# Kernel tuning notes

Hardware: AMD Instinct MI355X
Metric: run time of the kernel (lower is better)

The kernel has to match this reference:

```python
import jax, jax.numpy as jnp
import numpy as np

B, S, HID = 2, 2048, 2048
H, KVH, D = 8, 1, 256
RQ, RK, RV = 6, 2, 2
SCALING = 256 ** -0.5  # query_pre_attn_scalar
SOFTCAP = 50.0
NEG = -2.3819763e38


def setup_inputs() -> dict:
    key = jax.random.key(0)
    ks = jax.random.split(key, 9)
    hidden_states = jax.random.normal(ks[0], (B, S, HID), dtype=jnp.float32)
    # RoPE tables (split-half convention, matching torch view_as_complex path)
    inv_freq = 1.0 / (10000.0 ** (np.arange(0, D, 2, dtype=np.float32) / D))
    t = np.arange(S, dtype=np.float32)
    ang = np.outer(t, inv_freq)  # [S, D/2]
    freqs_cos = jnp.asarray(np.cos(ang))
    freqs_sin = jnp.asarray(np.sin(ang))
    causal = jnp.tril(jnp.ones((S, S), dtype=bool))
    mask = jnp.where(causal, 0.0, NEG)[None, None].astype(jnp.float32)
    kv_write_indices = jnp.arange(S, dtype=jnp.int32)
    sc = lambda fan_in: 1.0 / np.sqrt(fan_in)
    W_A_q = jax.random.normal(ks[1], (H * RQ, HID), dtype=jnp.float32) * sc(HID)
    W_A_k = jax.random.normal(ks[2], (KVH * RK, HID), dtype=jnp.float32) * sc(HID)
    W_A_v = jax.random.normal(ks[3], (KVH * RV, HID), dtype=jnp.float32) * sc(HID)
    W_B_q = jax.random.normal(ks[4], (RQ * D, HID), dtype=jnp.float32) * sc(HID)
    W_B_k = jax.random.normal(ks[5], (RK * D, HID), dtype=jnp.float32) * sc(HID)
    W_B_v = jax.random.normal(ks[6], (RV * D, HID), dtype=jnp.float32) * sc(HID)
    W_o = jax.random.normal(ks[7], (HID, H * D), dtype=jnp.float32) * sc(H * D)
    return {"hidden_states": hidden_states, "freqs_cos": freqs_cos,
            "freqs_sin": freqs_sin, "mask": mask,
            "kv_write_indices": kv_write_indices,
            "W_A_q": W_A_q, "W_A_k": W_A_k, "W_A_v": W_A_v,
            "W_B_q": W_B_q, "W_B_k": W_B_k, "W_B_v": W_B_v, "W_o": W_o}


def _rope(x, cos, sin):
    # x: [B,S,R,D]; cos/sin: [S,D/2]. Split-half rotation.
    x1, x2 = jnp.split(x, 2, axis=-1)
    c = cos[None, :, None, :]
    s = sin[None, :, None, :]
    return jnp.concatenate([x1 * c - x2 * s, x1 * s + x2 * c], axis=-1)


def reference(hidden_states, freqs_cos, freqs_sin, mask, kv_write_indices,
              W_A_q, W_A_k, W_A_v, W_B_q, W_B_k, W_B_v, W_o):
    b, s, _ = hidden_states.shape
    A_q = (hidden_states @ W_A_q.T).reshape(b, s, H, RQ)
    A_k = (hidden_states @ W_A_k.T).reshape(b, s, KVH, RK)
    A_v = (hidden_states @ W_A_v.T).reshape(b, s, KVH, RV)
    B_q = (hidden_states @ W_B_q.T).reshape(b, s, RQ, D)
    B_k = (hidden_states @ W_B_k.T).reshape(b, s, RK, D)
    B_v = (hidden_states @ W_B_v.T).reshape(b, s, RV, D)
    B_q = _rope(B_q, freqs_cos, freqs_sin)
    B_k = _rope(B_k, freqs_cos, freqs_sin)
    # Prefill: kv_write_indices = arange(s), so cache slices equal current factors.
    # GQA expansion of KV A-factors to all heads.
    A_k = jnp.repeat(A_k, H // KVH, axis=2)  # [b,s,H,RK]
    A_v = jnp.repeat(A_v, H // KVH, axis=2)
    # Reconstruct full-rank Q/K/V from TPA factors (1/rank per TPA definition).
    q = jnp.einsum('bshr,bsrd->bshd', A_q, B_q) / RQ
    k = jnp.einsum('bshr,bsrd->bshd', A_k, B_k) / RK
    v = jnp.einsum('bshr,bsrd->bshd', A_v, B_v) / RV
    scores = jnp.einsum('bqhd,bkhd->bhqk', q, k) * SCALING
    scores = jnp.tanh(scores / SOFTCAP) * SOFTCAP
    scores = scores + mask
    probs = jax.nn.softmax(scores.astype(jnp.float32), axis=-1).astype(q.dtype)
    out = jnp.einsum('bhqk,bkhd->bqhd', probs, v).reshape(b, s, H * D)
    return out @ W_o.T
```

## Files before the change

kernel.cpp:

```cpp
#include <hip/hip_runtime.h>
#include <hip/hip_bf16.h>
#include <stdint.h>

typedef __bf16 bf16;
typedef __bf16 bf16x8 __attribute__((ext_vector_type(8)));
typedef float  f32x4  __attribute__((ext_vector_type(4)));

static constexpr int S_LEN = 2048;
static constexpr int HIDN  = 2048;
static constexpr int BATCH = 2;
static constexpr int MTOT  = BATCH * S_LEN;
static constexpr int NH    = 8;
static constexpr int DH    = 256;
static constexpr int NPAD  = 2688;
static constexpr float QSCALE = 0.0625f / 6.0f;

__device__ __forceinline__ void gload16(const bf16* g, const bf16* l) {
  __builtin_amdgcn_global_load_lds(
      (const __attribute__((address_space(1))) void*)g,
      (__attribute__((address_space(3))) void*)l, 16, 0, 0);
}

__global__ void cast_x_kernel(const float* __restrict__ in, bf16* __restrict__ out) {
  int i = blockIdx.x * blockDim.x + threadIdx.x;
  const float4* p = reinterpret_cast<const float4*>(in) + 2 * (size_t)i;
  float4 a = p[0], b = p[1];
  bf16x8 o;
  o[0]=(bf16)a.x; o[1]=(bf16)a.y; o[2]=(bf16)a.z; o[3]=(bf16)a.w;
  o[4]=(bf16)b.x; o[5]=(bf16)b.y; o[6]=(bf16)b.z; o[7]=(bf16)b.w;
  reinterpret_cast<bf16x8*>(out)[i] = o;
}

__global__ void cast_w_kernel(const float* __restrict__ Wq, const float* __restrict__ Wk,
                              const float* __restrict__ Wv, const float* __restrict__ Bq,
                              const float* __restrict__ Bk, const float* __restrict__ Bv,
                              const float* __restrict__ Wo, bf16* __restrict__ Wcat,
                              bf16* __restrict__ Wob) {
  int row = blockIdx.x;
  int c = threadIdx.x * 8;
  const float* src = nullptr;
  bf16* dst;
  if (row < NPAD) {
    dst = Wcat + (size_t)row * HIDN;
    if      (row <   48) src = Wq + (size_t)row        * HIDN;
    else if (row <   50) src = Wk + (size_t)(row-  48) * HIDN;
    else if (row <   52) src = Wv + (size_t)(row-  50) * HIDN;
    else if (row < 1588) src = Bq + (size_t)(row-  52) * HIDN;
    else if (row < 2100) src = Bk + (size_t)(row-1588) * HIDN;
    else if (row < 2612) src = Bv + (size_t)(row-2100) * HIDN;
  } else {
    dst = Wob + (size_t)(row - NPAD) * HIDN;
    src = Wo + (size_t)(row - NPAD) * HIDN;
  }
  bf16x8 o;
  if (src) {
    const float4* p = reinterpret_cast<const float4*>(src + c);
    float4 a = p[0], b = p[1];
    o[0]=(bf16)a.x; o[1]=(bf16)a.y; o[2]=(bf16)a.z; o[3]=(bf16)a.w;
    o[4]=(bf16)b.x; o[5]=(bf16)b.y; o[6]=(bf16)b.z; o[7]=(bf16)b.w;
  } else {
    #pragma unroll
    for (int j = 0; j < 8; ++j) o[j] = (bf16)0.f;
  }
  *reinterpret_cast<bf16x8*>(dst + c) = o;
}

__launch_bounds__(256)
__global__ void gemm_bt_kernel(const bf16* __restrict__ A, const bf16* __restrict__ Bt,
                               float* __restrict__ C, int K, int N) {
  __shared__ __align__(16) bf16 As[2][128 * 64];
  __shared__ __align__(16) bf16 Bs[2][128 * 64];
  const int t = threadIdx.x;
  const int lane = t & 63, wid = t >> 6;
  const int g = lane >> 4, c16 = lane & 15;
  const int nwg = (int)(gridDim.x * gridDim.y);
  int flat = (int)(blockIdx.y * gridDim.x + blockIdx.x);
  flat = (flat & 7) * (nwg >> 3) + (flat >> 3);
  const int bxs = flat % (int)gridDim.x, bys = flat / (int)gridDim.x;
  const int rowA0 = bys * 128, rowB0 = bxs * 128;
  const int wrow = (wid >> 1) * 64, wcol = (wid & 1) * 64;
  const int srow = (lane >> 3), sunit = lane & 7;
  const int sgx = (sunit ^ (srow & 7)) * 8;
  const int rswz = c16 & 7;
  f32x4 z = {0.f, 0.f, 0.f, 0.f};
  f32x4 acc[4][4];
  #pragma unroll
  for (int m = 0; m < 4; ++m)
    #pragma unroll
    for (int n = 0; n < 4; ++n) acc[m][n] = z;

  auto stage = [&](int buf, int kt) {
    #pragma unroll
    for (int i = 0; i < 4; ++i) {
      int r0 = wid * 32 + i * 8;
      gload16(A + (size_t)(rowA0 + r0 + srow) * K + kt + sgx, &As[buf][r0 * 64]);
      gload16(Bt + (size_t)(rowB0 + r0 + srow) * K + kt + sgx, &Bs[buf][r0 * 64]);
    }
  };

  const int nk = K >> 6;
  stage(0, 0);
  __syncthreads();
  for (int ti = 0; ti < nk; ++ti) {
    const int cb = ti & 1;
    if (ti + 1 < nk) stage(cb ^ 1, (ti + 1) * 64);
    #pragma unroll
    for (int ks = 0; ks < 2; ++ks) {
      bf16x8 af[4], bfr[4];
      #pragma unroll
      for (int m = 0; m < 4; ++m)
        af[m] = *reinterpret_cast<const bf16x8*>(
            &As[cb][(wrow + m*16 + c16) * 64 + ((ks*4 + g) ^ rswz) * 8]);
      #pragma unroll
      for (int n = 0; n < 4; ++n)
        bfr[n] = *reinterpret_cast<const bf16x8*>(
            &Bs[cb][(wcol + n*16 + c16) * 64 + ((ks*4 + g) ^ rswz) * 8]);
      __builtin_amdgcn_s_setprio(1);
      #pragma unroll
      for (int m = 0; m < 4; ++m)
        #pragma unroll
        for (int n = 0; n < 4; ++n)
          acc[m][n] = __builtin_amdgcn_mfma_f32_16x16x32_bf16(af[m], bfr[n], acc[m][n], 0, 0, 0);
      __builtin_amdgcn_s_setprio(0);
    }
    __syncthreads();
  }
  #pragma unroll
  for (int m = 0; m < 4; ++m)
    #pragma unroll
    for (int n = 0; n < 4; ++n)
      #pragma unroll
      for (int r = 0; r < 4; ++r) {
        int row = rowA0 + wrow + m*16 + g*4 + r;
        int col = rowB0 + wcol + n*16 + c16;
        C[(size_t)row * N + col] = acc[m][n][r];
      }
}

__global__ void qkv_kernel(const float* __restrict__ P, const float* __restrict__ fcos,
                           const float* __restrict__ fsin, bf16* __restrict__ qat,
                           bf16* __restrict__ kat, bf16* __restrict__ vT) {
  const int m = blockIdx.x;
  const int b = m >> 11, s = m & 2047;
  const int d = threadIdx.x;
  __shared__ float Aq[48]; __shared__ float Ak[2]; __shared__ float Av[2];
  const float* Prow = P + (size_t)m * NPAD;
  if (d < 48) Aq[d] = Prow[d];
  else if (d < 50) Ak[d - 48] = Prow[d];
  else if (d < 52) Av[d - 50] = Prow[d];
  __syncthreads();
  const int dh = d & 127;
  const float co = fcos[s * 128 + dh], si = fsin[s * 128 + dh];
  const bool lo = (d < 128);
  float rq[6];
  #pragma unroll
  for (int r = 0; r < 6; ++r) {
    const float* Bq = Prow + 52 + r * 256;
    float x  = Bq[d];
    float xp = Bq[lo ? d + 128 : d - 128];
    rq[r] = lo ? (x * co - xp * si) : (xp * si + x * co);
  }
  #pragma unroll
  for (int h = 0; h < 8; ++h) {
    float a = 0.f;
    #pragma unroll
    for (int r = 0; r < 6; ++r) a += Aq[h * 6 + r] * rq[r];
    qat[((size_t)(b * 8 + h) * S_LEN + s) * DH + d] = (bf16)(a * QSCALE);
  }
  float ka = 0.f;
  #pragma unroll
  for (int r = 0; r < 2; ++r) {
    const float* Bk = Prow + 1588 + r * 256;
    float x  = Bk[d];
    float xp = Bk[lo ? d + 128 : d - 128];
    float rk = lo ? (x * co - xp * si) : (xp * si + x * co);
    ka += Ak[r] * rk;
  }
  kat[((size_t)b * S_LEN + s) * DH + d] = (bf16)(ka * 0.5f);
  float va = 0.f;
  #pragma unroll
  for (int r = 0; r < 2; ++r) va += Av[r] * Prow[2100 + r * 256 + d];
  vT[((size_t)b * DH + d) * S_LEN + s] = (bf16)(va * 0.5f);
}

__launch_bounds__(512)
__global__ void attn_kernel(const bf16* __restrict__ qat, const bf16* __restrict__ kat,
                            const bf16* __restrict__ vT, bf16* __restrict__ O) {
  const int pr = (int)blockIdx.x;
  const int bh = (int)blockIdx.y;
  const int b = bh >> 3, h8 = bh & 7;
  const int t = threadIdx.x, lane = t & 63, w = t >> 6;
  const int g = lane >> 4, c16 = lane & 15;
  const int rw = w & 3, hf = w >> 2;
  __shared__ __align__(16) bf16 Kb[2][64 * 256];
  __shared__ __align__(16) bf16 Vb[2][256 * 64];
  __shared__ __align__(16) bf16 Pl[8][16 * 40];
  __shared__ f32x4 Lc[4][64];
  float* Fc = (float*)&Kb[0][0];

  const int ks_r = lane >> 5, ks_x = lane & 31;
  const int vs_r = lane >> 3, vs_x = lane & 7;
  const size_t kbase = (size_t)b * S_LEN * DH;
  const size_t vbase = (size_t)b * DH * S_LEN;

  auto stage = [&](int buf, int j0) {
    #pragma unroll
    for (int i = 0; i < 4; ++i) {
      int lr = w * 8 + i * 2 + ks_r;
      int gx = ks_x ^ (lr & 7);
      gload16(kat + kbase + (size_t)(j0 + lr) * DH + gx * 8,
              &Kb[buf][(w * 8 + i * 2) * 256]);
    }
    #pragma unroll
    for (int i = 0; i < 4; ++i) {
      int lr = w * 32 + i * 8 + vs_r;
      int gx = vs_x ^ (lr & 7);
      gload16(vT + vbase + (size_t)lr * S_LEN + j0 + gx * 8,
              &Vb[buf][(w * 32 + i * 8) * 64]);
    }
  };

  f32x4 z = {0.f, 0.f, 0.f, 0.f};
  const int kswz = c16 & 7;

  #pragma unroll 1
  for (int half = 0; half < 2; ++half) {
    const int qt = half ? pr : 31 - pr;
    const int q0 = qt * 64;
    const int rowg0 = q0 + rw * 16 + g * 4;

    bf16x8 qf[8];
    {
      const bf16* qrow = qat + ((size_t)bh * S_LEN + q0 + rw * 16 + c16) * DH;
      #pragma unroll
      for (int kf = 0; kf < 8; ++kf)
        qf[kf] = *reinterpret_cast<const bf16x8*>(qrow + kf * 32 + g * 8);
    }
    f32x4 accO[16];
    #pragma unroll
    for (int i = 0; i < 16; ++i) accO[i] = z;
    float lr4[4] = {0.f, 0.f, 0.f, 0.f};

    const int nst = qt + 1;
    stage(0, 0);
    __syncthreads();

    for (int ts = 0; ts < nst; ++ts) {
      const int cb = ts & 1, nb = cb ^ 1;
      const int j0 = ts * 64;
      if (ts + 1 < nst) stage(nb, j0 + 64);

      f32x4 sc[2];
      #pragma unroll
      for (int nt = 0; nt < 2; ++nt) {
        f32x4 a = z;
        const int rk = hf * 32 + nt * 16 + c16;
        __builtin_amdgcn_s_setprio(1);
        #pragma unroll
        for (int kf = 0; kf < 8; ++kf) {
          bf16x8 kb = *reinterpret_cast<const bf16x8*>(
              &Kb[cb][rk * 256 + ((kf * 4 + g) ^ kswz) * 8]);
          a = __builtin_amdgcn_mfma_f32_16x16x32_bf16(qf[kf], kb, a, 0, 0, 0);
        }
        __builtin_amdgcn_s_setprio(0);
        sc[nt] = a;
      }
      #pragma unroll
      for (int nt = 0; nt < 2; ++nt) {
        int col = j0 + hf * 32 + nt * 16 + c16;
        #pragma unroll
        for (int r = 0; r < 4; ++r) {
          float x = sc[nt][r];
          float e2 = __expf(x * 0.04f);
          float p = (col <= rowg0 + r)
                      ? __expf(-100.f * __frcp_rn(e2 + 1.f))
                      : 0.f;
          lr4[r] += p;
          Pl[w][(g * 4 + r) * 40 + nt * 16 + c16] = (bf16)p;
        }
      }
      bf16x8 pa = *reinterpret_cast<const bf16x8*>(&Pl[w][c16 * 40 + g * 8]);
      __builtin_amdgcn_s_setprio(1);
      #pragma unroll
      for (int dt = 0; dt < 16; ++dt) {
        int vrow = dt * 16 + c16;
        bf16x8 vb = *reinterpret_cast<const bf16x8*>(
            &Vb[cb][vrow * 64 + ((hf * 4 + g) ^ (vrow & 7)) * 8]);
        accO[dt] = __builtin_amdgcn_mfma_f32_16x16x32_bf16(pa, vb, accO[dt], 0, 0, 0);
      }
      __builtin_amdgcn_s_setprio(0);
      __syncthreads();
    }

    if (hf == 1) {
      #pragma unroll
      for (int dt = 0; dt < 16; ++dt)
        #pragma unroll
        for (int r = 0; r < 4; ++r)
          Fc[rw * 4096 + (g * 4 + r) * 256 + dt * 16 + c16] = accO[dt][r];
      f32x4 lv = {lr4[0], lr4[1], lr4[2], lr4[3]};
      Lc[rw][lane] = lv;
    }
    __syncthreads();
    if (hf == 0) {
      f32x4 lo = Lc[rw][lane];
      #pragma unroll
      for (int r = 0; r < 4; ++r) lr4[r] += lo[r];
      #pragma unroll
      for (int dt = 0; dt < 16; ++dt)
        #pragma unroll
        for (int r = 0; r < 4; ++r)
          accO[dt][r] += Fc[rw * 4096 + (g * 4 + r) * 256 + dt * 16 + c16];
      #pragma unroll
      for (int r = 0; r < 4; ++r) {
        float l = lr4[r];
        l += __shfl_xor(l, 1);
        l += __shfl_xor(l, 2);
        l += __shfl_xor(l, 4);
        l += __shfl_xor(l, 8);
        float inv = 1.f / l;
        #pragma unroll
        for (int dt = 0; dt < 16; ++dt)
          O[((size_t)b * S_LEN + rowg0 + r) * (size_t)(NH * DH) + h8 * DH + dt * 16 + c16] =
              (bf16)(accO[dt][r] * inv);
      }
    }
    __syncthreads();
  }
}

extern "C" void kernel_launch(void* const* d_in, const int* in_sizes, int n_in,
                              void* d_out, int out_size, void* d_ws, size_t ws_size,
                              hipStream_t stream) {
  (void)in_sizes; (void)n_in; (void)out_size; (void)ws_size;
  const float* hs   = (const float*)d_in[0];
  const float* fcos = (const float*)d_in[1];
  const float* fsin = (const float*)d_in[2];
  const float* Wq = (const float*)d_in[5];
  const float* Wk = (const float*)d_in[6];
  const float* Wv = (const float*)d_in[7];
  const float* Bq = (const float*)d_in[8];
  const float* Bk = (const float*)d_in[9];
  const float* Bv = (const float*)d_in[10];
  const float* Wo = (const float*)d_in[11];

  char* ws = (char*)d_ws;
  size_t off = 0;
  auto alloc = [&](size_t bytes) {
    void* p = ws + off;
    off += (bytes + 255) & ~(size_t)255;
    return p;
  };
  bf16*  Xbf  = (bf16*) alloc((size_t)MTOT * HIDN * 2);
  bf16*  Wcat = (bf16*) alloc((size_t)NPAD * HIDN * 2);
  bf16*  Wob  = (bf16*) alloc((size_t)HIDN * HIDN * 2);
  float* P    = (float*)alloc((size_t)MTOT * NPAD * 4);
  bf16*  qat  = (bf16*) alloc((size_t)BATCH * NH * S_LEN * DH * 2);
  bf16*  kat  = (bf16*) alloc((size_t)BATCH * S_LEN * DH * 2);
  bf16*  vT   = (bf16*) alloc((size_t)BATCH * DH * S_LEN * 2);
  bf16*  Oat  = (bf16*) alloc((size_t)MTOT * NH * DH * 2);
  float* out  = (float*)d_out;

  cast_x_kernel<<<dim3(MTOT * HIDN / 8 / 256), dim3(256), 0, stream>>>(hs, Xbf);
  cast_w_kernel<<<dim3(NPAD + HIDN), dim3(256), 0, stream>>>(Wq, Wk, Wv, Bq, Bk, Bv, Wo, Wcat, Wob);
  gemm_bt_kernel<<<dim3(NPAD / 128, MTOT / 128), dim3(256), 0, stream>>>(Xbf, Wcat, P, HIDN, NPAD);
  qkv_kernel<<<dim3(MTOT), dim3(256), 0, stream>>>(P, fcos, fsin, qat, kat, vT);
  attn_kernel<<<dim3(16, BATCH * NH), dim3(512), 0, stream>>>(qat, kat, vT, Oat);
  gemm_bt_kernel<<<dim3(HIDN / 128, MTOT / 128), dim3(256), 0, stream>>>(Oat, Wob, out, HIDN, HIDN);
}
```

Baseline: 230.6 us.

## Restructure attention to 32x32 MFMA tiles with single-buffer 256-thread blocks

Rewrites the attention kernel so each block handles one 64-row query tile with 4 waves using 32x32x16 MFMAs instead of 16x16x32. P is moved between lanes with cross-half shuffles rather than an LDS round trip. The K/V double buffering is dropped in favour of a single buffer, and the grid is flattened to 512 blocks ordered longest-first, with launch bounds set for 2 blocks per CU. This aims to cut LDS traffic, remove the paired-tile scheduling, and raise occupancy, at the cost of no longer overlapping loads with compute inside a block.

Result: slower. 248.8 us (+7.9%).

```diff
diff --git a/kernel.cpp b/kernel.cpp
--- a/kernel.cpp
+++ b/kernel.cpp
@@ -5,6 +5,9 @@
 typedef __bf16 bf16;
 typedef __bf16 bf16x8 __attribute__((ext_vector_type(8)));
 typedef float  f32x4  __attribute__((ext_vector_type(4)));
+typedef float  f32x16 __attribute__((ext_vector_type(16)));
+typedef unsigned int u32;
+typedef u32 u32x4 __attribute__((ext_vector_type(4)));
 
 static constexpr int S_LEN = 2048;
 static constexpr int HIDN  = 2048;
@@ -183,149 +186,140 @@
   vT[((size_t)b * DH + d) * S_LEN + s] = (bf16)(va * 0.5f);
 }
 
-__launch_bounds__(512)
+__launch_bounds__(256, 2)
 __global__ void attn_kernel(const bf16* __restrict__ qat, const bf16* __restrict__ kat,
                             const bf16* __restrict__ vT, bf16* __restrict__ O) {
-  const int pr = (int)blockIdx.x;
-  const int bh = (int)blockIdx.y;
+  const int f = (int)blockIdx.x;
+  int qt, bh;
+  if (f < 256) { qt = 31 - (f & 31); bh = f >> 5; }
+  else         { int g2 = f - 256; qt = g2 & 31; bh = 8 + (g2 >> 5); }
   const int b = bh >> 3, h8 = bh & 7;
   const int t = threadIdx.x, lane = t & 63, w = t >> 6;
-  const int g = lane >> 4, c16 = lane & 15;
-  const int rw = w & 3, hf = w >> 2;
-  __shared__ __align__(16) bf16 Kb[2][64 * 256];
-  __shared__ __align__(16) bf16 Vb[2][256 * 64];
-  __shared__ __align__(16) bf16 Pl[8][16 * 40];
-  __shared__ f32x4 Lc[4][64];
-  float* Fc = (float*)&Kb[0][0];
-
-  const int ks_r = lane >> 5, ks_x = lane & 31;
-  const int vs_r = lane >> 3, vs_x = lane & 7;
+  const int l31 = lane & 31, hi = lane >> 5;
+  const int rg = w >> 1, hf = w & 1;
+  const int q0 = qt * 64;
+
+  __shared__ __align__(16) bf16 Kb[64 * 256];
+  __shared__ __align__(16) bf16 Vb[256 * 64];
+  __shared__ float Lh[2][32];
+  __shared__ float Li[2][32];
+
+  const int qrow = q0 + rg * 32 + l31;
+  bf16x8 qf[16];
+  {
+    const bf16* qp = qat + ((size_t)bh * S_LEN + qrow) * DH + hi * 8;
+    #pragma unroll
+    for (int kf = 0; kf < 16; ++kf)
+      qf[kf] = *reinterpret_cast<const bf16x8*>(qp + kf * 16);
+  }
+  f32x16 acc[8];
+  #pragma unroll
+  for (int dt = 0; dt < 8; ++dt)
+    #pragma unroll
+    for (int e = 0; e < 16; ++e) acc[dt][e] = 0.f;
+  float lsum = 0.f;
+
   const size_t kbase = (size_t)b * S_LEN * DH;
   const size_t vbase = (size_t)b * DH * S_LEN;
-
-  auto stage = [&](int buf, int j0) {
-    #pragma unroll
-    for (int i = 0; i < 4; ++i) {
-      int lr = w * 8 + i * 2 + ks_r;
-      int gx = ks_x ^ (lr & 7);
-      gload16(kat + kbase + (size_t)(j0 + lr) * DH + gx * 8,
-              &Kb[buf][(w * 8 + i * 2) * 256]);
-    }
-    #pragma unroll
-    for (int i = 0; i < 4; ++i) {
-      int lr = w * 32 + i * 8 + vs_r;
-      int gx = vs_x ^ (lr & 7);
-      gload16(vT + vbase + (size_t)lr * S_LEN + j0 + gx * 8,
-              &Vb[buf][(w * 32 + i * 8) * 64]);
-    }
-  };
-
-  f32x4 z = {0.f, 0.f, 0.f, 0.f};
-  const int kswz = c16 & 7;
-
-  #pragma unroll 1
-  for (int half = 0; half < 2; ++half) {
-    const int qt = half ? pr : 31 - pr;
-    const int q0 = qt * 64;
-    const int rowg0 = q0 + rw * 16 + g * 4;
-
-    bf16x8 qf[8];
-    {
-      const bf16* qrow = qat + ((size_t)bh * S_LEN + q0 + rw * 16 + c16) * DH;
-      #pragma unroll
-      for (int kf = 0; kf < 8; ++kf)
-        qf[kf] = *reinterpret_cast<const bf16x8*>(qrow + kf * 32 + g * 8);
-    }
-    f32x4 accO[16];
-    #pragma unroll
-    for (int i = 0; i < 16; ++i) accO[i] = z;
-    float lr4[4] = {0.f, 0.f, 0.f, 0.f};
-
-    const int nst = qt + 1;
-    stage(0, 0);
+  const int krow_rd = hf * 32 + l31;
+  const int kswz = l31 & 7;
+
+  for (int ts = 0; ts <= qt; ++ts) {
+    const int j0 = ts * 64;
+    #pragma unroll
+    for (int i = 0; i < 8; ++i) {
+      int kr = i * 8 + (t >> 5);
+      gload16(kat + kbase + (size_t)(j0 + kr) * DH + ((t & 31) ^ (kr & 7)) * 8,
+              &Kb[(i * 256 + w * 64) * 8]);
+      int vr = i * 32 + (t >> 3);
+      gload16(vT + vbase + (size_t)vr * S_LEN + j0 + ((t & 7) ^ (vr & 7)) * 8,
+              &Vb[(i * 256 + w * 64) * 8]);
+    }
     __syncthreads();
 
-    for (int ts = 0; ts < nst; ++ts) {
-      const int cb = ts & 1, nb = cb ^ 1;
-      const int j0 = ts * 64;
-      if (ts + 1 < nst) stage(nb, j0 + 64);
-
-      f32x4 sc[2];
-      #pragma unroll
-      for (int nt = 0; nt < 2; ++nt) {
-        f32x4 a = z;
-        const int rk = hf * 32 + nt * 16 + c16;
-        __builtin_amdgcn_s_setprio(1);
-        #pragma unroll
-        for (int kf = 0; kf < 8; ++kf) {
-          bf16x8 kb = *reinterpret_cast<const bf16x8*>(
-              &Kb[cb][rk * 256 + ((kf * 4 + g) ^ kswz) * 8]);
-          a = __builtin_amdgcn_mfma_f32_16x16x32_bf16(qf[kf], kb, a, 0, 0, 0);
-        }
-        __builtin_amdgcn_s_setprio(0);
-        sc[nt] = a;
+    f32x16 d0, d1;
+    #pragma unroll
+    for (int e = 0; e < 16; ++e) { d0[e] = 0.f; d1[e] = 0.f; }
+    __builtin_amdgcn_s_setprio(1);
+    #pragma unroll
+    for (int kf = 0; kf < 16; kf += 2) {
+      bf16x8 kb0 = *reinterpret_cast<const bf16x8*>(
+          &Kb[krow_rd * 256 + (((kf << 1) | hi) ^ kswz) * 8]);
+      d0 = __builtin_amdgcn_mfma_f32_32x32x16_bf16(kb0, qf[kf], d0, 0, 0, 0);
+      bf16x8 kb1 = *reinterpret_cast<const bf16x8*>(
+          &Kb[krow_rd * 256 + ((((kf + 1) << 1) | hi) ^ kswz) * 8]);
+      d1 = __builtin_amdgcn_mfma_f32_32x32x16_bf16(kb1, qf[kf + 1], d1, 0, 0, 0);
+    }
+    __builtin_amdgcn_s_setprio(0);
+
+    float p[16];
+    #pragma unroll
+    for (int r = 0; r < 16; ++r) {
+      int kv = j0 + hf * 32 + (r & 3) + ((r >> 2) << 3) + (hi << 2);
+      float x = d0[r] + d1[r];
+      float pv = (kv <= qrow)
+                   ? __expf(-100.f * __frcp_rn(__expf(x * 0.04f) + 1.f))
+                   : 0.f;
+      p[r] = pv;
+      lsum += pv;
+    }
+
+    u32 own[8], sw[8];
+    #pragma unroll
+    for (int j = 0; j < 8; ++j) {
+      unsigned short a = __builtin_bit_cast(unsigned short, (bf16)p[2 * j]);
+      unsigned short c = __builtin_bit_cast(unsigned short, (bf16)p[2 * j + 1]);
+      own[j] = (u32)a | ((u32)c << 16);
+    }
+    #pragma unroll
+    for (int j = 0; j < 8; ++j) sw[j] = (u32)__shfl_xor((int)own[j], 32);
+    u32x4 fa0 = hi ? u32x4{sw[2], sw[3], own[2], own[3]}
+                   : u32x4{own[0], own[1], sw[0], sw[1]};
+    u32x4 fa1 = hi ? u32x4{sw[6], sw[7], own[6], own[7]}
+                   : u32x4{own[4], own[5], sw[4], sw[5]};
+    bf16x8 pa0 = __builtin_bit_cast(bf16x8, fa0);
+    bf16x8 pa1 = __builtin_bit_cast(bf16x8, fa1);
+
+    __builtin_amdgcn_s_setprio(1);
+    #pragma unroll
+    for (int dt = 0; dt < 8; ++dt) {
+      int vrow = dt * 32 + l31;
+      bf16x8 vb0 = *reinterpret_cast<const bf16x8*>(
+          &Vb[vrow * 64 + (((hf << 2) | hi) ^ (vrow & 7)) * 8]);
+      acc[dt] = __builtin_amdgcn_mfma_f32_32x32x16_bf16(pa0, vb0, acc[dt], 0, 0, 0);
+      bf16x8 vb1 = *reinterpret_cast<const bf16x8*>(
+          &Vb[vrow * 64 + (((hf << 2) | 2 | hi) ^ (vrow & 7)) * 8]);
+      acc[dt] = __builtin_amdgcn_mfma_f32_32x32x16_bf16(pa1, vb1, acc[dt], 0, 0, 0);
+    }
+    __builtin_amdgcn_s_setprio(0);
+    __syncthreads();
+  }
+
+  lsum += __shfl_xor(lsum, 32);
+  float* Fc = (rg == 0) ? (float*)Kb : (float*)Vb;
+  if (hf == 1) {
+    #pragma unroll
+    for (int dt = 0; dt < 8; ++dt)
+      #pragma unroll
+      for (int r = 0; r < 16; ++r) {
+        int ql = (r & 3) + ((r >> 2) << 3) + (hi << 2);
+        Fc[ql * 256 + dt * 32 + l31] = acc[dt][r];
       }
-      #pragma unroll
-      for (int nt = 0; nt < 2; ++nt) {
-        int col = j0 + hf * 32 + nt * 16 + c16;
-        #pragma unroll
-        for (int r = 0; r < 4; ++r) {
-          float x = sc[nt][r];
-          float e2 = __expf(x * 0.04f);
-          float p = (col <= rowg0 + r)
-                      ? __expf(-100.f * __frcp_rn(e2 + 1.f))
-                      : 0.f;
-          lr4[r] += p;
-          Pl[w][(g * 4 + r) * 40 + nt * 16 + c16] = (bf16)p;
-        }
+    if (lane < 32) Lh[rg][l31] = lsum;
+  }
+  __syncthreads();
+  if (hf == 0) {
+    float ltot = lsum + Lh[rg][l31];
+    if (lane < 32) Li[rg][l31] = 1.f / ltot;
+    #pragma unroll
+    for (int dt = 0; dt < 8; ++dt)
+      #pragma unroll
+      for (int r = 0; r < 16; ++r) {
+        int ql = (r & 3) + ((r >> 2) << 3) + (hi << 2);
+        float v = (acc[dt][r] + Fc[ql * 256 + dt * 32 + l31]) * Li[rg][ql];
+        O[((size_t)b * S_LEN + q0 + rg * 32 + ql) * (size_t)(NH * DH) + h8 * DH +
+          dt * 32 + l31] = (bf16)v;
       }
-      bf16x8 pa = *reinterpret_cast<const bf16x8*>(&Pl[w][c16 * 40 + g * 8]);
-      __builtin_amdgcn_s_setprio(1);
-      #pragma unroll
-      for (int dt = 0; dt < 16; ++dt) {
-        int vrow = dt * 16 + c16;
-        bf16x8 vb = *reinterpret_cast<const bf16x8*>(
-            &Vb[cb][vrow * 64 + ((hf * 4 + g) ^ (vrow & 7)) * 8]);
-        accO[dt] = __builtin_amdgcn_mfma_f32_16x16x32_bf16(pa, vb, accO[dt], 0, 0, 0);
-      }
-      __builtin_amdgcn_s_setprio(0);
-      __syncthreads();
-    }
-
-    if (hf == 1) {
-      #pragma unroll
-      for (int dt = 0; dt < 16; ++dt)
-        #pragma unroll
-        for (int r = 0; r < 4; ++r)
-          Fc[rw * 4096 + (g * 4 + r) * 256 + dt * 16 + c16] = accO[dt][r];
-      f32x4 lv = {lr4[0], lr4[1], lr4[2], lr4[3]};
-      Lc[rw][lane] = lv;
-    }
-    __syncthreads();
-    if (hf == 0) {
-      f32x4 lo = Lc[rw][lane];
-      #pragma unroll
-      for (int r = 0; r < 4; ++r) lr4[r] += lo[r];
-      #pragma unroll
-      for (int dt = 0; dt < 16; ++dt)
-        #pragma unroll
-        for (int r = 0; r < 4; ++r)
-          accO[dt][r] += Fc[rw * 4096 + (g * 4 + r) * 256 + dt * 16 + c16];
-      #pragma unroll
-      for (int r = 0; r < 4; ++r) {
-        float l = lr4[r];
-        l += __shfl_xor(l, 1);
-        l += __shfl_xor(l, 2);
-        l += __shfl_xor(l, 4);
-        l += __shfl_xor(l, 8);
-        float inv = 1.f / l;
-        #pragma unroll
-        for (int dt = 0; dt < 16; ++dt)
-          O[((size_t)b * S_LEN + rowg0 + r) * (size_t)(NH * DH) + h8 * DH + dt * 16 + c16] =
-              (bf16)(accO[dt][r] * inv);
-      }
-    }
-    __syncthreads();
   }
 }
 
@@ -365,6 +359,6 @@
   cast_w_kernel<<<dim3(NPAD + HIDN), dim3(256), 0, stream>>>(Wq, Wk, Wv, Bq, Bk, Bv, Wo, Wcat, Wob);
   gemm_bt_kernel<<<dim3(NPAD / 128, MTOT / 128), dim3(256), 0, stream>>>(Xbf, Wcat, P, HIDN, NPAD);
   qkv_kernel<<<dim3(MTOT), dim3(256), 0, stream>>>(P, fcos, fsin, qat, kat, vT);
-  attn_kernel<<<dim3(16, BATCH * NH), dim3(512), 0, stream>>>(qat, kat, vT, Oat);
+  attn_kernel<<<dim3(512), dim3(256), 0, stream>>>(qat, kat, vT, Oat);
   gemm_bt_kernel<<<dim3(HIDN / 128, MTOT / 128), dim3(256), 0, stream>>>(Oat, Wob, out, HIDN, HIDN);
 }
```

## Single-buffer K/V in attention, split query-tile pairs into separate blocks

Applied to the files above, without the earlier changes.

The attention kernel stops pairing two query tiles per block and launches one block per query tile, with the heavy tiles (the first 256 block indices) scheduled before the light ones. The double-buffered K and V LDS tiles are replaced by one shared buffer. The next K tile is prefetched after QK^T and the next V tile after PV, each behind a barrier, and launch bounds request more resident blocks. This trades the prefetch overlap of double buffering for lower LDS use and higher occupancy, plus more, finer-grained blocks for load balance across CUs.

Result: slower. 393.5 us (+70.7%).

```diff
diff --git a/kernel.cpp b/kernel.cpp
--- a/kernel.cpp
+++ b/kernel.cpp
@@ -183,149 +183,153 @@
   vT[((size_t)b * DH + d) * S_LEN + s] = (bf16)(va * 0.5f);
 }
 
-__launch_bounds__(512)
+__launch_bounds__(512, 4)
 __global__ void attn_kernel(const bf16* __restrict__ qat, const bf16* __restrict__ kat,
                             const bf16* __restrict__ vT, bf16* __restrict__ O) {
-  const int pr = (int)blockIdx.x;
-  const int bh = (int)blockIdx.y;
+  const int f = (int)blockIdx.x;
+  const int u = f & 255;
+  const int pq = u & 15;
+  const int bh = u >> 4;
+  const int qt = (f < 256) ? (31 - pq) : pq;
   const int b = bh >> 3, h8 = bh & 7;
   const int t = threadIdx.x, lane = t & 63, w = t >> 6;
   const int g = lane >> 4, c16 = lane & 15;
   const int rw = w & 3, hf = w >> 2;
-  __shared__ __align__(16) bf16 Kb[2][64 * 256];
-  __shared__ __align__(16) bf16 Vb[2][256 * 64];
+  const int q0 = qt * 64;
+
+  __shared__ __align__(16) bf16 KVb[64 * 256 + 256 * 64];
   __shared__ __align__(16) bf16 Pl[8][16 * 40];
   __shared__ f32x4 Lc[4][64];
-  float* Fc = (float*)&Kb[0][0];
+  bf16* Kb = KVb;
+  bf16* Vb = KVb + 64 * 256;
+  float* Fc = (float*)KVb;
 
   const int ks_r = lane >> 5, ks_x = lane & 31;
   const int vs_r = lane >> 3, vs_x = lane & 7;
   const size_t kbase = (size_t)b * S_LEN * DH;
   const size_t vbase = (size_t)b * DH * S_LEN;
 
-  auto stage = [&](int buf, int j0) {
+  auto stageK = [&](int j0) {
     #pragma unroll
     for (int i = 0; i < 4; ++i) {
       int lr = w * 8 + i * 2 + ks_r;
       int gx = ks_x ^ (lr & 7);
       gload16(kat + kbase + (size_t)(j0 + lr) * DH + gx * 8,
-              &Kb[buf][(w * 8 + i * 2) * 256]);
-    }
+              &Kb[(w * 8 + i * 2) * 256]);
+    }
+  };
+  auto stageV = [&](int j0) {
     #pragma unroll
     for (int i = 0; i < 4; ++i) {
       int lr = w * 32 + i * 8 + vs_r;
       int gx = vs_x ^ (lr & 7);
       gload16(vT + vbase + (size_t)lr * S_LEN + j0 + gx * 8,
-              &Vb[buf][(w * 32 + i * 8) * 64]);
+              &Vb[(w * 32 + i * 8) * 64]);
     }
   };
 
   f32x4 z = {0.f, 0.f, 0.f, 0.f};
   const int kswz = c16 & 7;
-
-  #pragma unroll 1
-  for (int half = 0; half < 2; ++half) {
-    const int qt = half ? pr : 31 - pr;
-    const int q0 = qt * 64;
-    const int rowg0 = q0 + rw * 16 + g * 4;
-
-    bf16x8 qf[8];
-    {
-      const bf16* qrow = qat + ((size_t)bh * S_LEN + q0 + rw * 16 + c16) * DH;
-      #pragma unroll
-      for (int kf = 0; kf < 8; ++kf)
-        qf[kf] = *reinterpret_cast<const bf16x8*>(qrow + kf * 32 + g * 8);
-    }
-    f32x4 accO[16];
-    #pragma unroll
-    for (int i = 0; i < 16; ++i) accO[i] = z;
-    float lr4[4] = {0.f, 0.f, 0.f, 0.f};
-
-    const int nst = qt + 1;
-    stage(0, 0);
-    __syncthreads();
-
-    for (int ts = 0; ts < nst; ++ts) {
-      const int cb = ts & 1, nb = cb ^ 1;
-      const int j0 = ts * 64;
-      if (ts + 1 < nst) stage(nb, j0 + 64);
-
-      f32x4 sc[2];
-      #pragma unroll
-      for (int nt = 0; nt < 2; ++nt) {
-        f32x4 a = z;
-        const int rk = hf * 32 + nt * 16 + c16;
-        __builtin_amdgcn_s_setprio(1);
-        #pragma unroll
-        for (int kf = 0; kf < 8; ++kf) {
-          bf16x8 kb = *reinterpret_cast<const bf16x8*>(
-              &Kb[cb][rk * 256 + ((kf * 4 + g) ^ kswz) * 8]);
-          a = __builtin_amdgcn_mfma_f32_16x16x32_bf16(qf[kf], kb, a, 0, 0, 0);
-        }
-        __builtin_amdgcn_s_setprio(0);
-        sc[nt] = a;
-      }
-      #pragma unroll
-      for (int nt = 0; nt < 2; ++nt) {
-        int col = j0 + hf * 32 + nt * 16 + c16;
-        #pragma unroll
-        for (int r = 0; r < 4; ++r) {
-          float x = sc[nt][r];
-          float e2 = __expf(x * 0.04f);
-          float p = (col <= rowg0 + r)
-                      ? __expf(-100.f * __frcp_rn(e2 + 1.f))
-                      : 0.f;
-          lr4[r] += p;
-          Pl[w][(g * 4 + r) * 40 + nt * 16 + c16] = (bf16)p;
-        }
-      }
-      bf16x8 pa = *reinterpret_cast<const bf16x8*>(&Pl[w][c16 * 40 + g * 8]);
+  const int rowg0 = q0 + rw * 16 + g * 4;
+
+  bf16x8 qf[8];
+  {
+    const bf16* qrow = qat + ((size_t)bh * S_LEN + q0 + rw * 16 + c16) * DH;
+    #pragma unroll
+    for (int kf = 0; kf < 8; ++kf)
+      qf[kf] = *reinterpret_cast<const bf16x8*>(qrow + kf * 32 + g * 8);
+  }
+  f32x4 accO[16];
+  #pragma unroll
+  for (int i = 0; i < 16; ++i) accO[i] = z;
+  float lr4[4] = {0.f, 0.f, 0.f, 0.f};
+
+  const int nst = qt + 1;
+  stageK(0);
+  stageV(0);
+  __syncthreads();
+
+  for (int ts = 0; ts < nst; ++ts) {
+    const int j0 = ts * 64;
+
+    f32x4 sc[2];
+    #pragma unroll
+    for (int nt = 0; nt < 2; ++nt) {
+      f32x4 a = z;
+      const int rk = hf * 32 + nt * 16 + c16;
       __builtin_amdgcn_s_setprio(1);
       #pragma unroll
-      for (int dt = 0; dt < 16; ++dt) {
-        int vrow = dt * 16 + c16;
-        bf16x8 vb = *reinterpret_cast<const bf16x8*>(
-            &Vb[cb][vrow * 64 + ((hf * 4 + g) ^ (vrow & 7)) * 8]);
-        accO[dt] = __builtin_amdgcn_mfma_f32_16x16x32_bf16(pa, vb, accO[dt], 0, 0, 0);
+      for (int kf = 0; kf < 8; ++kf) {
+        bf16x8 kb = *reinterpret_cast<const bf16x8*>(
+            &Kb[rk * 256 + ((kf * 4 + g) ^ kswz) * 8]);
+        a = __builtin_amdgcn_mfma_f32_16x16x32_bf16(qf[kf], kb, a, 0, 0, 0);
       }
       __builtin_amdgcn_s_setprio(0);
-      __syncthreads();
-    }
-
-    if (hf == 1) {
+      sc[nt] = a;
+    }
+    __syncthreads();
+    if (ts + 1 < nst) stageK(j0 + 64);
+
+    #pragma unroll
+    for (int nt = 0; nt < 2; ++nt) {
+      int col = j0 + hf * 32 + nt * 16 + c16;
+      #pragma unroll
+      for (int r = 0; r < 4; ++r) {
+        float x = sc[nt][r];
+        float e2 = __expf(x * 0.04f);
+        float p = (col <= rowg0 + r)
+                    ? __expf(-100.f * __frcp_rn(e2 + 1.f))
+                    : 0.f;
+        lr4[r] += p;
+        Pl[w][(g * 4 + r) * 40 + nt * 16 + c16] = (bf16)p;
+      }
+    }
+    bf16x8 pa = *reinterpret_cast<const bf16x8*>(&Pl[w][c16 * 40 + g * 8]);
+    __builtin_amdgcn_s_setprio(1);
+    #pragma unroll
+    for (int dt = 0; dt < 16; ++dt) {
+      int vrow = dt * 16 + c16;
+      bf16x8 vb = *reinterpret_cast<const bf16x8*>(
+          &Vb[vrow * 64 + ((hf * 4 + g) ^ (vrow & 7)) * 8]);
+      accO[dt] = __builtin_amdgcn_mfma_f32_16x16x32_bf16(pa, vb, accO[dt], 0, 0, 0);
+    }
+    __builtin_amdgcn_s_setprio(0);
+    __syncthreads();
+    if (ts + 1 < nst) stageV(j0 + 64);
+  }
+
+  if (hf == 1) {
+    #pragma unroll
+    for (int dt = 0; dt < 16; ++dt)
+      #pragma unroll
+      for (int r = 0; r < 4; ++r)
+        Fc[rw * 4096 + (g * 4 + r) * 256 + dt * 16 + c16] = accO[dt][r];
+    f32x4 lv = {lr4[0], lr4[1], lr4[2], lr4[3]};
+    Lc[rw][lane] = lv;
+  }
+  __syncthreads();
+  if (hf == 0) {
+    f32x4 lo = Lc[rw][lane];
+    #pragma unroll
+    for (int r = 0; r < 4; ++r) lr4[r] += lo[r];
+    #pragma unroll
+    for (int dt = 0; dt < 16; ++dt)
+      #pragma unroll
+      for (int r = 0; r < 4; ++r)
+        accO[dt][r] += Fc[rw * 4096 + (g * 4 + r) * 256 + dt * 16 + c16];
+    #pragma unroll
+    for (int r = 0; r < 4; ++r) {
+      float l = lr4[r];
+      l += __shfl_xor(l, 1);
+      l += __shfl_xor(l, 2);
+      l += __shfl_xor(l, 4);
+      l += __shfl_xor(l, 8);
+      float inv = 1.f / l;
       #pragma unroll
       for (int dt = 0; dt < 16; ++dt)
-        #pragma unroll
-        for (int r = 0; r < 4; ++r)
-          Fc[rw * 4096 + (g * 4 + r) * 256 + dt * 16 + c16] = accO[dt][r];
-      f32x4 lv = {lr4[0], lr4[1], lr4[2], lr4[3]};
-      Lc[rw][lane] = lv;
-    }
-    __syncthreads();
-    if (hf == 0) {
-      f32x4 lo = Lc[rw][lane];
-      #pragma unroll
-      for (int r = 0; r < 4; ++r) lr4[r] += lo[r];
-      #pragma unroll
-      for (int dt = 0; dt < 16; ++dt)
-        #pragma unroll
-        for (int r = 0; r < 4; ++r)
-          accO[dt][r] += Fc[rw * 4096 + (g * 4 + r) * 256 + dt * 16 + c16];
-      #pragma unroll
-      for (int r = 0; r < 4; ++r) {
-        float l = lr4[r];
-        l += __shfl_xor(l, 1);
-        l += __shfl_xor(l, 2);
-        l += __shfl_xor(l, 4);
-        l += __shfl_xor(l, 8);
-        float inv = 1.f / l;
-        #pragma unroll
-        for (int dt = 0; dt < 16; ++dt)
-          O[((size_t)b * S_LEN + rowg0 + r) * (size_t)(NH * DH) + h8 * DH + dt * 16 + c16] =
-              (bf16)(accO[dt][r] * inv);
-      }
-    }
-    __syncthreads();
+        O[((size_t)b * S_LEN + rowg0 + r) * (size_t)(NH * DH) + h8 * DH + dt * 16 + c16] =
+            (bf16)(accO[dt][r] * inv);
+    }
   }
 }
 
@@ -365,6 +369,6 @@
   cast_w_kernel<<<dim3(NPAD + HIDN), dim3(256), 0, stream>>>(Wq, Wk, Wv, Bq, Bk, Bv, Wo, Wcat, Wob);
   gemm_bt_kernel<<<dim3(NPAD / 128, MTOT / 128), dim3(256), 0, stream>>>(Xbf, Wcat, P, HIDN, NPAD);
   qkv_kernel<<<dim3(MTOT), dim3(256), 0, stream>>>(P, fcos, fsin, qat, kat, vT);
-  attn_kernel<<<dim3(16, BATCH * NH), dim3(512), 0, stream>>>(qat, kat, vT, Oat);
+  attn_kernel<<<dim3(512), dim3(512), 0, stream>>>(qat, kat, vT, Oat);
   gemm_bt_kernel<<<dim3(HIDN / 128, MTOT / 128), dim3(256), 0, stream>>>(Oat, Wob, out, HIDN, HIDN);
 }
```
